# Optimization experiments

Hardware: AMD Instinct MI355X
Metric: run time of the kernel (lower is better)

Reference implementation:

```python
import jax, jax.numpy as jnp
import numpy as np

B, D, H4, L, T, VOCAB, DMID = 256, 512, 2048, 3, 201, 128, 1024
START_IDX = 0


def setup_inputs() -> dict:
    key = jax.random.key(0)
    ks = jax.random.split(key, 8)
    s = lambda k, shape, scale=0.02: jax.random.normal(k, shape, jnp.float32) * scale
    return {
        "feat": jax.random.normal(ks[0], (B, D), jnp.float32),
        "Wvis": s(ks[1], (D, D)),
        "bvis": jnp.zeros((D,), jnp.float32),
        "embed": s(ks[2], (VOCAB, D)),
        "Wih": s(ks[3], (L, H4, D)),
        "Whh": s(ks[4], (L, H4, D)),
        "bih": jnp.zeros((L, H4), jnp.float32),
        "bhh": jnp.zeros((L, H4), jnp.float32),
        "W1": s(ks[5], (DMID, D)),
        "b1": jnp.zeros((DMID,), jnp.float32),
        "W2": s(ks[6], (VOCAB, DMID)),
        "b2": jnp.zeros((VOCAB,), jnp.float32),
    }


def reference(feat, Wvis, bvis, embed, Wih, Whh, bih, bhh, W1, b1, W2, b2):
    # visual_proj applied once in forward(), then again per-layer in _init_hidden
    feat_p = feat @ Wvis.T + bvis                    # [B,D]
    h0_layer = feat_p @ Wvis.T + bvis                # same for every layer
    h0 = jnp.tile(h0_layer[None], (L, 1, 1))         # [L,B,D]
    c0 = jnp.zeros_like(h0)
    inp0 = jnp.broadcast_to(embed[START_IDX], (B, D))  # embed(<sos>)

    def step(carry, _):
        inp, h, c = carry
        x = inp
        hs, cs = [], []
        for l in range(L):  # small fixed layer count
            g = x @ Wih[l].T + bih[l] + h[l] @ Whh[l].T + bhh[l]  # [B,4D]
            i, f, gg, o = jnp.split(g, 4, axis=-1)  # torch gate order i,f,g,o
            c_l = jax.nn.sigmoid(f) * c[l] + jax.nn.sigmoid(i) * jnp.tanh(gg)
            h_l = jax.nn.sigmoid(o) * jnp.tanh(c_l)
            hs.append(h_l)
            cs.append(c_l)
            x = h_l
        out = x  # top-layer output; dropout is identity in eval
        # inp = out.detach() in the original loop
        return (jax.lax.stop_gradient(out), jnp.stack(hs), jnp.stack(cs)), out

    _, outs = jax.lax.scan(step, (inp0, h0, c0), None, length=T)  # [T,B,D]
    res = outs.transpose(1, 0, 2)                                 # [B,T,D]
    mid = jax.nn.gelu(res @ W1.T + b1, approximate=False)         # torch GELU is erf-exact
    logits = mid @ W2.T + b2                                      # [B,T,V]
    return logits.transpose(0, 2, 1)                              # [B,V,T]
```

## Files before the change

kernel.cpp:

```cpp
#include <hip/hip_runtime.h>

#define NB   256
#define ND   512
#define NH4  2048
#define NL   3
#define NT   201
#define NV   128
#define NMID 1024

typedef _Float16 half8 __attribute__((ext_vector_type(8)));
typedef float f32x4 __attribute__((ext_vector_type(4)));

__device__ __forceinline__ float sigf(float x) { return 1.0f / (1.0f + __expf(-x)); }
__device__ __forceinline__ float tanh_(float x) {
  float e = __expf(-2.0f * fabsf(x));
  float t = (1.0f - e) / (1.0f + e);
  return x < 0.0f ? -t : t;
}

__device__ __forceinline__ half8 l2_load(const _Float16* p) {
  half8 v;
  asm volatile("global_load_dwordx4 %0, %1, off sc0" : "=v"(v) : "v"(p));
  return v;
}

__device__ __forceinline__ unsigned l2_rmw_add(unsigned* p, unsigned val) {
  unsigned v;
  asm volatile("global_atomic_add %0, %1, %2, off sc0\n\ts_waitcnt vmcnt(0)"
               : "=v"(v) : "v"(p), "v"(val) : "memory");
  return v;
}

__device__ __forceinline__ void xbar(unsigned* cnt, bool pref) {
  if (pref && threadIdx.x >= 256)
    asm volatile("s_waitcnt vmcnt(8)" ::: "memory");
  else
    asm volatile("s_waitcnt vmcnt(0)" ::: "memory");
  __syncthreads();
  if (threadIdx.x == 0) {
    unsigned old = l2_rmw_add(cnt, 1u);
    unsigned target = (old & ~31u) + 32u;
    int guard = 1 << 16;
    while (l2_rmw_add(cnt, 0u) < target && --guard)
      __builtin_amdgcn_s_sleep(2);
  }
  __syncthreads();
  asm volatile("buffer_inv" ::: "memory");
  __builtin_amdgcn_sched_barrier(0);
}

__global__ void prep_all(const float* __restrict__ Wih, const float* __restrict__ Whh,
                         const float* __restrict__ bih, const float* __restrict__ bhh,
                         const float* __restrict__ Wvis, const float* __restrict__ feat,
                         const float* __restrict__ embed, const float* __restrict__ W1,
                         const float* __restrict__ W2,
                         _Float16* __restrict__ Wp, float* __restrict__ bp,
                         _Float16* __restrict__ Wvis16, _Float16* __restrict__ feat16,
                         _Float16* __restrict__ x0, _Float16* __restrict__ W1h,
                         _Float16* __restrict__ W2h, unsigned* __restrict__ cnt) {
  size_t idx = (size_t)blockIdx.x * 256 + threadIdx.x;
  {
    int k = (int)(idx & 1023);
    int R = (int)((idx >> 10) & 2047);
    int l = (int)(idx >> 21);
    int dt = R >> 6, g = (R >> 4) & 3, di = R & 15;
    int col = g * 512 + dt * 16 + di;
    float v = (k < 512) ? Wih[((size_t)l * NH4 + col) * ND + k]
                        : Whh[((size_t)l * NH4 + col) * ND + (k - 512)];
    Wp[idx] = (_Float16)v;
  }
  if (idx < (size_t)NL * NH4) {
    int R = (int)(idx & 2047);
    int l = (int)(idx >> 11);
    int dt = R >> 6, g = (R >> 4) & 3, di = R & 15;
    int col = g * 512 + dt * 16 + di;
    bp[idx] = bih[l * NH4 + col] + bhh[l * NH4 + col];
  }
  if (idx < 512 * 512)  Wvis16[idx] = (_Float16)Wvis[idx];
  if (idx < 256 * 512)  feat16[idx] = (_Float16)feat[idx];
  if (idx < 256 * 512)  x0[idx]     = (_Float16)embed[idx & 511];
  if (idx < 1024 * 512) W1h[idx]    = (_Float16)W1[idx];
  if (idx < 128 * 1024) W2h[idx]    = (_Float16)W2[idx];
  if (idx < 1024) cnt[idx] = 0;
}

__global__ __launch_bounds__(512, 2) void lstm_persist(
    const _Float16* __restrict__ Wp,
    const float* __restrict__ bp,
    const _Float16* __restrict__ Wvis,
    const float* __restrict__ bvis,
    const _Float16* __restrict__ feat16,
    const _Float16* __restrict__ x0,
    _Float16* __restrict__ featp,
    _Float16* __restrict__ hbuf,
    _Float16* __restrict__ res,
    unsigned* __restrict__ cntbase) {
  __shared__ _Float16 wlds[64][1024];
  __shared__ float expart[4][32][16][4];

  const int tid = threadIdx.x;
  const int lane = tid & 63, w = tid >> 6;
  const int lr = lane & 15, lg = (lane >> 4) & 3;

  unsigned xcd;
  asm volatile("s_getreg_b32 %0, hwreg(HW_REG_XCC_ID)" : "=s"(xcd));
  xcd &= 7u;

  unsigned* rank_slot = (unsigned*)&expart[0][0][0][0];
  if (tid == 0)
    *rank_slot = __hip_atomic_fetch_add(cntbase + 256 + xcd * 32, 1u,
                                        __ATOMIC_RELAXED, __HIP_MEMORY_SCOPE_AGENT);
  __syncthreads();
  const int rank = (int)(*rank_slot & 31u);
  __syncthreads();

  const int dt = rank;
  const int m0 = (int)xcd * 32;
  const int d0 = rank * 16;
  unsigned* cnt = cntbase + xcd * 32;

  #pragma unroll 4
  for (int i = 0; i < 16; ++i) {
    int G = tid + 512 * i;
    int r = G >> 7, g = G & 127;
    *(half8*)&wlds[r][(g ^ (r & 7)) * 8] =
        *(const half8*)(Wp + ((size_t)(dt * 64 + r)) * 1024 + g * 8);
  }
  half8 wreg[2][4][4];
  #pragma unroll
  for (int ly = 0; ly < 2; ++ly)
    #pragma unroll
    for (int n = 0; n < 4; ++n)
      #pragma unroll
      for (int kk = 0; kk < 4; ++kk)
        wreg[ly][n][kk] = *(const half8*)(Wp +
          ((size_t)((ly + 1) * NH4 + dt * 64 + n * 16 + lr)) * 1024 + w * 128 + kk * 32 + lg * 8);

  const int di = tid & 15, cb = (tid >> 4) & 31;
  f32x4 breg4[3];
  #pragma unroll
  for (int l = 0; l < 3; ++l)
    #pragma unroll
    for (int g = 0; g < 4; ++g)
      breg4[l][g] = bp[l * NH4 + dt * 64 + g * 16 + di];

  {
    float* xb = &expart[0][0][0][0];
    const int wm2 = w & 1, wk = w >> 1;
    #pragma unroll 1
    for (int pg = 0; pg < 2; ++pg) {
      const _Float16* A = pg ? featp : feat16;
      half8 avp[4];
      #pragma unroll
      for (int kc = 0; kc < 4; ++kc)
        avp[kc] = l2_load(A + (size_t)(m0 + wm2 * 16 + lr) * ND + wk * 128 + kc * 32 + lg * 8);
      asm volatile("s_waitcnt vmcnt(0)" ::: "memory");
      __builtin_amdgcn_sched_barrier(0);
      f32x4 pacc = {0.f, 0.f, 0.f, 0.f};
      #pragma unroll
      for (int kc = 0; kc < 4; ++kc) {
        half8 bb = *(const half8*)(Wvis + (size_t)(d0 + lr) * ND + wk * 128 + kc * 32 + lg * 8);
        pacc = __builtin_amdgcn_mfma_f32_16x16x32_f16(avp[kc], bb, pacc, 0, 0, 0);
      }
      #pragma unroll
      for (int j = 0; j < 4; ++j)
        xb[wk * 512 + (wm2 * 16 + lg * 4 + j) * 16 + lr] = pacc[j];
      __syncthreads();
      {
        int m = tid >> 4, d = tid & 15;
        float v = xb[m * 16 + d] + xb[512 + m * 16 + d] + xb[1024 + m * 16 + d]
                + xb[1536 + m * 16 + d] + bvis[d0 + d];
        _Float16 hv = (_Float16)v;
        size_t off = (size_t)(m0 + m) * ND + d0 + d;
        if (pg == 0) featp[off] = hv;
        else {
          hbuf[(size_t)(0 * 2 + 1) * (NB * ND) + off] = hv;
          hbuf[(size_t)(1 * 2 + 1) * (NB * ND) + off] = hv;
          hbuf[(size_t)(2 * 2 + 1) * (NB * ND) + off] = hv;
        }
      }
      xbar(cnt, false);
    }
  }

  float cst[3] = {0.f, 0.f, 0.f};
  const size_t aoff0 = (size_t)(m0 + lr) * ND + (size_t)(w & 3) * 128 + lg * 8;
  const size_t aoff1 = aoff0 + (size_t)16 * ND;
  half8 av0[4], av1[4];

  #pragma unroll 1
  for (int t = 0; t < NT; ++t) {
    #pragma unroll
    for (int l = 0; l < 3; ++l) {
      const _Float16* xsrc = (l == 0)
        ? ((t == 0) ? x0 : hbuf + (size_t)(2 * 2 + ((t + 1) & 1)) * (NB * ND))
        : hbuf + (size_t)((l - 1) * 2 + (t & 1)) * (NB * ND);
      const _Float16* hsrc = hbuf + (size_t)(l * 2 + ((t + 1) & 1)) * (NB * ND);
      _Float16* hdst       = hbuf + (size_t)(l * 2 + (t & 1)) * (NB * ND);

      f32x4 acc[2][4];
      #pragma unroll
      for (int m = 0; m < 2; ++m)
        #pragma unroll
        for (int n = 0; n < 4; ++n)
          acc[m][n] = (f32x4){0.f, 0.f, 0.f, 0.f};

      if (w < 4) {
        #pragma unroll
        for (int kk = 0; kk < 4; ++kk) {
          av0[kk] = l2_load(xsrc + aoff0 + kk * 32);
          av1[kk] = l2_load(xsrc + aoff1 + kk * 32);
        }
        asm volatile("s_waitcnt vmcnt(4)"
                     : "+v"(av0[0]), "+v"(av0[1]), "+v"(av1[0]), "+v"(av1[1]));
        __builtin_amdgcn_s_setprio(1);
        #pragma unroll
        for (int kk = 0; kk < 2; ++kk)
          #pragma unroll
          for (int n = 0; n < 4; ++n) {
            half8 bf;
            if (l == 0) {
              int kg = w * 16 + kk * 4 + lg;
              bf = *(const half8*)&wlds[n * 16 + lr][(kg ^ (lr & 7)) * 8];
            } else bf = wreg[l - 1][n][kk];
            acc[0][n] = __builtin_amdgcn_mfma_f32_16x16x32_f16(av0[kk], bf, acc[0][n], 0, 0, 0);
            acc[1][n] = __builtin_amdgcn_mfma_f32_16x16x32_f16(av1[kk], bf, acc[1][n], 0, 0, 0);
          }
        __builtin_amdgcn_s_setprio(0);
        asm volatile("s_waitcnt vmcnt(0)"
                     : "+v"(av0[2]), "+v"(av0[3]), "+v"(av1[2]), "+v"(av1[3]));
        __builtin_amdgcn_s_setprio(1);
        #pragma unroll
        for (int kk = 2; kk < 4; ++kk)
          #pragma unroll
          for (int n = 0; n < 4; ++n) {
            half8 bf;
            if (l == 0) {
              int kg = w * 16 + kk * 4 + lg;
              bf = *(const half8*)&wlds[n * 16 + lr][(kg ^ (lr & 7)) * 8];
            } else bf = wreg[l - 1][n][kk];
            acc[0][n] = __builtin_amdgcn_mfma_f32_16x16x32_f16(av0[kk], bf, acc[0][n], 0, 0, 0);
            acc[1][n] = __builtin_amdgcn_mfma_f32_16x16x32_f16(av1[kk], bf, acc[1][n], 0, 0, 0);
          }
        __builtin_amdgcn_s_setprio(0);
      } else {
        if (t == 0 && l == 0) {
          #pragma unroll
          for (int kk = 0; kk < 4; ++kk) {
            av0[kk] = l2_load(hsrc + aoff0 + kk * 32);
            av1[kk] = l2_load(hsrc + aoff1 + kk * 32);
          }
        }
        asm volatile("s_waitcnt vmcnt(0)"
                     : "+v"(av0[0]), "+v"(av0[1]), "+v"(av0[2]), "+v"(av0[3]),
                       "+v"(av1[0]), "+v"(av1[1]), "+v"(av1[2]), "+v"(av1[3]));
        __builtin_amdgcn_s_setprio(1);
        #pragma unroll
        for (int kk = 0; kk < 4; ++kk)
          #pragma unroll
          for (int n = 0; n < 4; ++n) {
            half8 bf;
            if (l == 0) {
              int kg = w * 16 + kk * 4 + lg;
              bf = *(const half8*)&wlds[n * 16 + lr][(kg ^ (lr & 7)) * 8];
            } else bf = wreg[l - 1][n][kk];
            acc[0][n] = __builtin_amdgcn_mfma_f32_16x16x32_f16(av0[kk], bf, acc[0][n], 0, 0, 0);
            acc[1][n] = __builtin_amdgcn_mfma_f32_16x16x32_f16(av1[kk], bf, acc[1][n], 0, 0, 0);
          }
        __builtin_amdgcn_s_setprio(0);
      }

      if (w >= 4) {
        #pragma unroll
        for (int m = 0; m < 2; ++m)
          #pragma unroll
          for (int j = 0; j < 4; ++j) {
            f32x4 v = {acc[m][0][j], acc[m][1][j], acc[m][2][j], acc[m][3][j]};
            *(f32x4*)&expart[w - 4][m * 16 + lg * 4 + j][lr][0] = v;
          }
      }
      __syncthreads();
      if (w < 4) {
        #pragma unroll
        for (int m = 0; m < 2; ++m)
          #pragma unroll
          for (int j = 0; j < 4; ++j) {
            f32x4* pp = (f32x4*)&expart[w][m * 16 + lg * 4 + j][lr][0];
            f32x4 tv = *pp;
            tv[0] += acc[m][0][j]; tv[1] += acc[m][1][j];
            tv[2] += acc[m][2][j]; tv[3] += acc[m][3][j];
            *pp = tv;
          }
      }
      __syncthreads();

      {
        f32x4 s4 = breg4[l];
        #pragma unroll
        for (int s = 0; s < 4; ++s) {
          f32x4 g = *(const f32x4*)&expart[s][cb][di][0];
          s4 += g;
        }
        float c = cst[l];
        c = sigf(s4[1]) * c + sigf(s4[0]) * tanh_(s4[2]);
        cst[l] = c;
        _Float16 hv = (_Float16)(sigf(s4[3]) * tanh_(c));
        size_t off = (size_t)(m0 + cb) * ND + d0 + di;
        hdst[off] = hv;
        if (l == 2) res[(size_t)t * (NB * ND) + off] = hv;
      }

      if (!(t == NT - 1 && l == 2)) {
        if (w >= 4) {
          const int nt2 = (l == 2) ? t + 1 : t;
          const int nl  = (l == 2) ? 0 : l + 1;
          const _Float16* nh = hbuf + (size_t)(nl * 2 + ((nt2 + 1) & 1)) * (NB * ND);
          #pragma unroll
          for (int kk = 0; kk < 4; ++kk) {
            av0[kk] = l2_load(nh + aoff0 + kk * 32);
            av1[kk] = l2_load(nh + aoff1 + kk * 32);
          }
        }
        xbar(cnt, true);
      }
    }
  }
}

__global__ __launch_bounds__(256, 2) void head_kernel(
    const _Float16* __restrict__ res,
    const _Float16* __restrict__ W1h,
    const float* __restrict__ b1,
    const _Float16* __restrict__ W2h,
    const float* __restrict__ b2,
    float* __restrict__ out) {
  const int tile = blockIdx.x;
  const int tid = threadIdx.x;
  const int lane = tid & 63, w = tid >> 6;
  const int lr = lane & 15, lg = lane >> 4;
  const int r0 = tile * 64;

  __shared__ _Float16 mid[64][128];

  f32x4 acc2[8];
  #pragma unroll
  for (int n = 0; n < 8; ++n) acc2[n] = (f32x4){0.f, 0.f, 0.f, 0.f};

  const size_t arow = (size_t)(r0 + w * 16 + lr) * ND;

  #pragma unroll 1
  for (int nc = 0; nc < 8; ++nc) {
    f32x4 acc1[8];
    #pragma unroll
    for (int n = 0; n < 8; ++n) acc1[n] = (f32x4){0.f, 0.f, 0.f, 0.f};
    #pragma unroll 2
    for (int kc = 0; kc < 16; ++kc) {
      half8 a = *(const half8*)(res + arow + kc * 32 + lg * 8);
      #pragma unroll
      for (int n = 0; n < 8; ++n) {
        half8 bb = *(const half8*)(W1h + (size_t)(nc * 128 + n * 16 + lr) * ND + kc * 32 + lg * 8);
        acc1[n] = __builtin_amdgcn_mfma_f32_16x16x32_f16(a, bb, acc1[n], 0, 0, 0);
      }
    }
    __syncthreads();
    #pragma unroll
    for (int n = 0; n < 8; ++n) {
      #pragma unroll
      for (int j = 0; j < 4; ++j) {
        int m = w * 16 + lg * 4 + j;
        int col = n * 16 + lr;
        float v = acc1[n][j] + b1[nc * 128 + col];
        v = 0.5f * v * (1.0f + erff(v * 0.7071067811865475f));
        int sw = (((col >> 3) ^ (m & 15)) << 3) + (col & 7);
        mid[m][sw] = (_Float16)v;
      }
    }
    __syncthreads();
    #pragma unroll
    for (int kc2 = 0; kc2 < 4; ++kc2) {
      int row = w * 16 + lr;
      int blk = (kc2 * 4 + lg) ^ (row & 15);
      half8 a2 = *(const half8*)(&mid[row][blk * 8]);
      #pragma unroll
      for (int n = 0; n < 8; ++n) {
        half8 bb = *(const half8*)(W2h + (size_t)(n * 16 + lr) * NMID + nc * 128 + kc2 * 32 + lg * 8);
        acc2[n] = __builtin_amdgcn_mfma_f32_16x16x32_f16(a2, bb, acc2[n], 0, 0, 0);
      }
    }
  }
  #pragma unroll
  for (int n = 0; n < 8; ++n) {
    #pragma unroll
    for (int j = 0; j < 4; ++j) {
      int r = r0 + w * 16 + lg * 4 + j;
      int b = r & 255, t = r >> 8;
      int v = n * 16 + lr;
      out[((size_t)b * NV + v) * NT + t] = acc2[n][j] + b2[v];
    }
  }
}

extern "C" void kernel_launch(void* const* d_in, const int* in_sizes, int n_in,
                              void* d_out, int out_size, void* d_ws, size_t ws_size,
                              hipStream_t stream) {
  const float* feat  = (const float*)d_in[0];
  const float* Wvis  = (const float*)d_in[1];
  const float* bvis  = (const float*)d_in[2];
  const float* embed = (const float*)d_in[3];
  const float* Wih   = (const float*)d_in[4];
  const float* Whh   = (const float*)d_in[5];
  const float* bih   = (const float*)d_in[6];
  const float* bhh   = (const float*)d_in[7];
  const float* W1    = (const float*)d_in[8];
  const float* b1    = (const float*)d_in[9];
  const float* W2    = (const float*)d_in[10];
  const float* b2    = (const float*)d_in[11];
  float* out = (float*)d_out;

  char* p = (char*)d_ws;
  _Float16* Wp     = (_Float16*)p; p += (size_t)NL * NH4 * 1024 * 2;
  _Float16* Wvis16 = (_Float16*)p; p += (size_t)512 * 512 * 2;
  _Float16* feat16 = (_Float16*)p; p += (size_t)256 * 512 * 2;
  _Float16* x0     = (_Float16*)p; p += (size_t)256 * 512 * 2;
  _Float16* featp  = (_Float16*)p; p += (size_t)256 * 512 * 2;
  _Float16* hbuf   = (_Float16*)p; p += (size_t)NL * 2 * NB * ND * 2;
  _Float16* resb   = (_Float16*)p; p += (size_t)NT * NB * ND * 2;
  _Float16* W1h    = (_Float16*)p; p += (size_t)NMID * ND * 2;
  _Float16* W2h    = (_Float16*)p; p += (size_t)NV * NMID * 2;
  float*    bp     = (float*)p;    p += (size_t)NL * NH4 * 4;
  unsigned* cnt    = (unsigned*)p; p += 4096;

  prep_all<<<24576, 256, 0, stream>>>(Wih, Whh, bih, bhh, Wvis, feat, embed, W1, W2,
                                      Wp, bp, Wvis16, feat16, x0, W1h, W2h, cnt);
  lstm_persist<<<256, 512, 0, stream>>>(Wp, bp, Wvis16, bvis, feat16, x0,
                                        featp, hbuf, resb, cnt);
  head_kernel<<<804, 256, 0, stream>>>(resb, W1h, b1, W2h, b2, out);
  (void)in_sizes; (void)n_in; (void)out_size; (void)ws_size;
}
```

Baseline: 2.829 ms.

## Relax grid-barrier waits, preload layer-0 LDS weights into registers, and back off early arrivals

The grid barrier is split so each caller chooses its own vmcnt wait. The res store now goes through inline asm so that store does not have to drain before the barrier (vmcnt 9 or 1 at layer 2). The first two k-chunks of the layer-0 weight fragments are read from LDS into registers before the barrier of the previous step, which hides LDS latency in the critical MFMA path. Blocks that arrive at the barrier early sleep briefly to cut atomic polling traffic on L2. The cost is more register pressure, and the early sleep may add latency.

```diff
diff --git a/kernel.cpp b/kernel.cpp
--- a/kernel.cpp
+++ b/kernel.cpp
@@ -31,15 +31,13 @@
   return v;
 }
 
-__device__ __forceinline__ void xbar(unsigned* cnt, bool pref) {
-  if (pref && threadIdx.x >= 256)
-    asm volatile("s_waitcnt vmcnt(8)" ::: "memory");
-  else
-    asm volatile("s_waitcnt vmcnt(0)" ::: "memory");
+__device__ __forceinline__ void xbar_core(unsigned* cnt) {
   __syncthreads();
   if (threadIdx.x == 0) {
     unsigned old = l2_rmw_add(cnt, 1u);
     unsigned target = (old & ~31u) + 32u;
+    int ahead = 31 - (int)(old & 31u);
+    if (ahead > 8) __builtin_amdgcn_s_sleep(8);
     int guard = 1 << 16;
     while (l2_rmw_add(cnt, 0u) < target && --guard)
       __builtin_amdgcn_s_sleep(2);
@@ -144,6 +142,8 @@
     for (int g = 0; g < 4; ++g)
       breg4[l][g] = bp[l * NH4 + dt * 64 + g * 16 + di];
 
+  half8 bl0[2][4];
+
   {
     float* xb = &expart[0][0][0][0];
     const int wm2 = w & 1, wk = w >> 1;
@@ -179,8 +179,19 @@
           hbuf[(size_t)(2 * 2 + 1) * (NB * ND) + off] = hv;
         }
       }
-      xbar(cnt, false);
-    }
+      asm volatile("s_waitcnt vmcnt(0)" ::: "memory");
+      xbar_core(cnt);
+    }
+  }
+
+  if (w < 4) {
+    #pragma unroll
+    for (int kk = 0; kk < 2; ++kk)
+      #pragma unroll
+      for (int n = 0; n < 4; ++n) {
+        int kg = w * 16 + kk * 4 + lg;
+        bl0[kk][n] = *(const half8*)&wlds[n * 16 + lr][(kg ^ (lr & 7)) * 8];
+      }
   }
 
   float cst[3] = {0.f, 0.f, 0.f};
@@ -216,6 +227,18 @@
         __builtin_amdgcn_s_setprio(1);
         #pragma unroll
         for (int kk = 0; kk < 2; ++kk)
+          #pragma unroll
+          for (int n = 0; n < 4; ++n) {
+            half8 bf = (l == 0) ? bl0[kk][n] : wreg[l - 1][n][kk];
+            acc[0][n] = __builtin_amdgcn_mfma_f32_16x16x32_f16(av0[kk], bf, acc[0][n], 0, 0, 0);
+            acc[1][n] = __builtin_amdgcn_mfma_f32_16x16x32_f16(av1[kk], bf, acc[1][n], 0, 0, 0);
+          }
+        __builtin_amdgcn_s_setprio(0);
+        asm volatile("s_waitcnt vmcnt(0)"
+                     : "+v"(av0[2]), "+v"(av0[3]), "+v"(av1[2]), "+v"(av1[3]));
+        __builtin_amdgcn_s_setprio(1);
+        #pragma unroll
+        for (int kk = 2; kk < 4; ++kk)
           #pragma unroll
           for (int n = 0; n < 4; ++n) {
             half8 bf;
@@ -227,11 +250,20 @@
             acc[1][n] = __builtin_amdgcn_mfma_f32_16x16x32_f16(av1[kk], bf, acc[1][n], 0, 0, 0);
           }
         __builtin_amdgcn_s_setprio(0);
+      } else {
+        if (t == 0 && l == 0) {
+          #pragma unroll
+          for (int kk = 0; kk < 4; ++kk) {
+            av0[kk] = l2_load(hsrc + aoff0 + kk * 32);
+            av1[kk] = l2_load(hsrc + aoff1 + kk * 32);
+          }
+        }
         asm volatile("s_waitcnt vmcnt(0)"
-                     : "+v"(av0[2]), "+v"(av0[3]), "+v"(av1[2]), "+v"(av1[3]));
+                     : "+v"(av0[0]), "+v"(av0[1]), "+v"(av0[2]), "+v"(av0[3]),
+                       "+v"(av1[0]), "+v"(av1[1]), "+v"(av1[2]), "+v"(av1[3]));
         __builtin_amdgcn_s_setprio(1);
         #pragma unroll
-        for (int kk = 2; kk < 4; ++kk)
+        for (int kk = 0; kk < 4; ++kk)
           #pragma unroll
           for (int n = 0; n < 4; ++n) {
             half8 bf;
@@ -243,31 +275,6 @@
             acc[1][n] = __builtin_amdgcn_mfma_f32_16x16x32_f16(av1[kk], bf, acc[1][n], 0, 0, 0);
           }
         __builtin_amdgcn_s_setprio(0);
-      } else {
-        if (t == 0 && l == 0) {
-          #pragma unroll
-          for (int kk = 0; kk < 4; ++kk) {
-            av0[kk] = l2_load(hsrc + aoff0 + kk * 32);
-            av1[kk] = l2_load(hsrc + aoff1 + kk * 32);
-          }
-        }
-        asm volatile("s_waitcnt vmcnt(0)"
-                     : "+v"(av0[0]), "+v"(av0[1]), "+v"(av0[2]), "+v"(av0[3]),
-                       "+v"(av1[0]), "+v"(av1[1]), "+v"(av1[2]), "+v"(av1[3]));
-        __builtin_amdgcn_s_setprio(1);
-        #pragma unroll
-        for (int kk = 0; kk < 4; ++kk)
-          #pragma unroll
-          for (int n = 0; n < 4; ++n) {
-            half8 bf;
-            if (l == 0) {
-              int kg = w * 16 + kk * 4 + lg;
-              bf = *(const half8*)&wlds[n * 16 + lr][(kg ^ (lr & 7)) * 8];
-            } else bf = wreg[l - 1][n][kk];
-            acc[0][n] = __builtin_amdgcn_mfma_f32_16x16x32_f16(av0[kk], bf, acc[0][n], 0, 0, 0);
-            acc[1][n] = __builtin_amdgcn_mfma_f32_16x16x32_f16(av1[kk], bf, acc[1][n], 0, 0, 0);
-          }
-        __builtin_amdgcn_s_setprio(0);
       }
 
       if (w >= 4) {
@@ -307,7 +314,12 @@
         _Float16 hv = (_Float16)(sigf(s4[3]) * tanh_(c));
         size_t off = (size_t)(m0 + cb) * ND + d0 + di;
         hdst[off] = hv;
-        if (l == 2) res[(size_t)t * (NB * ND) + off] = hv;
+        if (l == 2) {
+          unsigned hw = (unsigned)__builtin_bit_cast(unsigned short, hv);
+          _Float16* rp = res + (size_t)t * (NB * ND) + off;
+          asm volatile("global_store_short %0, %1, off"
+                       :: "v"(rp), "v"(hw) : "memory");
+        }
       }
 
       if (!(t == NT - 1 && l == 2)) {
@@ -320,8 +332,23 @@
             av0[kk] = l2_load(nh + aoff0 + kk * 32);
             av1[kk] = l2_load(nh + aoff1 + kk * 32);
           }
-        }
-        xbar(cnt, true);
+        } else if (l == 2) {
+          #pragma unroll
+          for (int kk = 0; kk < 2; ++kk)
+            #pragma unroll
+            for (int n = 0; n < 4; ++n) {
+              int kg = w * 16 + kk * 4 + lg;
+              bl0[kk][n] = *(const half8*)&wlds[n * 16 + lr][(kg ^ (lr & 7)) * 8];
+            }
+        }
+        if (l == 2) {
+          if (w >= 4) asm volatile("s_waitcnt vmcnt(9)" ::: "memory");
+          else        asm volatile("s_waitcnt vmcnt(1)" ::: "memory");
+        } else {
+          if (w >= 4) asm volatile("s_waitcnt vmcnt(8)" ::: "memory");
+          else        asm volatile("s_waitcnt vmcnt(0)" ::: "memory");
+        }
+        xbar_core(cnt);
       }
     }
   }
```

Result: slower. 3.260 ms (+15.2%).

## Retile head kernel so each wave computes a 64x64 block with register reuse

Applied to the files above, without the earlier changes.

The head GEMM kernel is restructured so that each wave computes all 64 rows against its own slice of the hidden dimension. Each loaded W1/W2 fragment is reused across 4 row tiles (4x4 MFMA blocks), where before each wave did 16 rows times 8 column tiles and every wave reloaded the whole weight set. The intermediate buffer grows to four per-wave 64x128 slabs (64KB of LDS), and the second GEMM splits the output columns across waves. The aim is to cut redundant global weight traffic in the head. The costs are higher register pressure, larger LDS use that may lower occupancy, and the fact that the head is likely a small share of total time next to the recurrent LSTM.

```diff
diff --git a/kernel.cpp b/kernel.cpp
--- a/kernel.cpp
+++ b/kernel.cpp
@@ -334,70 +334,93 @@
     const _Float16* __restrict__ W2h,
     const float* __restrict__ b2,
     float* __restrict__ out) {
-  const int tile = blockIdx.x;
   const int tid = threadIdx.x;
   const int lane = tid & 63, w = tid >> 6;
-  const int lr = lane & 15, lg = lane >> 4;
-  const int r0 = tile * 64;
-
-  __shared__ _Float16 mid[64][128];
-
-  f32x4 acc2[8];
+  const int lr = lane & 15, lg = (lane >> 4) & 3;
+  const int r0 = blockIdx.x * 64;
+
+  __shared__ _Float16 mid[4][64][128];
+
+  f32x4 acc2[4][2];
   #pragma unroll
-  for (int n = 0; n < 8; ++n) acc2[n] = (f32x4){0.f, 0.f, 0.f, 0.f};
-
-  const size_t arow = (size_t)(r0 + w * 16 + lr) * ND;
+  for (int m = 0; m < 4; ++m)
+    #pragma unroll
+    for (int n2 = 0; n2 < 2; ++n2) acc2[m][n2] = (f32x4){0.f, 0.f, 0.f, 0.f};
 
   #pragma unroll 1
-  for (int nc = 0; nc < 8; ++nc) {
-    f32x4 acc1[8];
-    #pragma unroll
-    for (int n = 0; n < 8; ++n) acc1[n] = (f32x4){0.f, 0.f, 0.f, 0.f};
-    #pragma unroll 2
-    for (int kc = 0; kc < 16; ++kc) {
-      half8 a = *(const half8*)(res + arow + kc * 32 + lg * 8);
-      #pragma unroll
-      for (int n = 0; n < 8; ++n) {
-        half8 bb = *(const half8*)(W1h + (size_t)(nc * 128 + n * 16 + lr) * ND + kc * 32 + lg * 8);
-        acc1[n] = __builtin_amdgcn_mfma_f32_16x16x32_f16(a, bb, acc1[n], 0, 0, 0);
-      }
+  for (int rr = 0; rr < 2; ++rr) {
+    const int c = rr * 4 + w;
+    #pragma unroll 1
+    for (int nh = 0; nh < 2; ++nh) {
+      f32x4 acc1[4][4];
+      #pragma unroll
+      for (int m = 0; m < 4; ++m)
+        #pragma unroll
+        for (int n = 0; n < 4; ++n) acc1[m][n] = (f32x4){0.f, 0.f, 0.f, 0.f};
+      #pragma unroll 2
+      for (int kc = 0; kc < 16; ++kc) {
+        half8 af[4];
+        #pragma unroll
+        for (int m = 0; m < 4; ++m)
+          af[m] = *(const half8*)(res + (size_t)(r0 + m * 16 + lr) * ND + kc * 32 + lg * 8);
+        #pragma unroll
+        for (int n = 0; n < 4; ++n) {
+          half8 bb = *(const half8*)(W1h +
+              (size_t)(c * 128 + nh * 64 + n * 16 + lr) * ND + kc * 32 + lg * 8);
+          #pragma unroll
+          for (int m = 0; m < 4; ++m)
+            acc1[m][n] = __builtin_amdgcn_mfma_f32_16x16x32_f16(af[m], bb, acc1[m][n], 0, 0, 0);
+        }
+      }
+      #pragma unroll
+      for (int n = 0; n < 4; ++n)
+        #pragma unroll
+        for (int m = 0; m < 4; ++m)
+          #pragma unroll
+          for (int j = 0; j < 4; ++j) {
+            int row = m * 16 + lg * 4 + j;
+            int col = nh * 64 + n * 16 + lr;
+            float v = acc1[m][n][j] + b1[c * 128 + col];
+            v = 0.5f * v * (1.0f + erff(v * 0.7071067811865475f));
+            int sw = (((col >> 3) ^ (row & 15)) << 3) + (col & 7);
+            mid[w][row][sw] = (_Float16)v;
+          }
     }
     __syncthreads();
-    #pragma unroll
-    for (int n = 0; n < 8; ++n) {
-      #pragma unroll
-      for (int j = 0; j < 4; ++j) {
-        int m = w * 16 + lg * 4 + j;
-        int col = n * 16 + lr;
-        float v = acc1[n][j] + b1[nc * 128 + col];
-        v = 0.5f * v * (1.0f + erff(v * 0.7071067811865475f));
-        int sw = (((col >> 3) ^ (m & 15)) << 3) + (col & 7);
-        mid[m][sw] = (_Float16)v;
+    #pragma unroll 1
+    for (int s = 0; s < 4; ++s) {
+      #pragma unroll
+      for (int kc2 = 0; kc2 < 4; ++kc2) {
+        half8 a2[4];
+        #pragma unroll
+        for (int m = 0; m < 4; ++m) {
+          int row = m * 16 + lr;
+          int blk = (kc2 * 4 + lg) ^ (row & 15);
+          a2[m] = *(const half8*)&mid[s][row][blk * 8];
+        }
+        #pragma unroll
+        for (int n2 = 0; n2 < 2; ++n2) {
+          half8 bb = *(const half8*)(W2h +
+              (size_t)(w * 32 + n2 * 16 + lr) * NMID + rr * 512 + s * 128 + kc2 * 32 + lg * 8);
+          #pragma unroll
+          for (int m = 0; m < 4; ++m)
+            acc2[m][n2] = __builtin_amdgcn_mfma_f32_16x16x32_f16(a2[m], bb, acc2[m][n2], 0, 0, 0);
+        }
       }
     }
     __syncthreads();
+  }
+  #pragma unroll
+  for (int n2 = 0; n2 < 2; ++n2)
     #pragma unroll
-    for (int kc2 = 0; kc2 < 4; ++kc2) {
-      int row = w * 16 + lr;
-      int blk = (kc2 * 4 + lg) ^ (row & 15);
-      half8 a2 = *(const half8*)(&mid[row][blk * 8]);
-      #pragma unroll
-      for (int n = 0; n < 8; ++n) {
-        half8 bb = *(const half8*)(W2h + (size_t)(n * 16 + lr) * NMID + nc * 128 + kc2 * 32 + lg * 8);
-        acc2[n] = __builtin_amdgcn_mfma_f32_16x16x32_f16(a2, bb, acc2[n], 0, 0, 0);
-      }
-    }
-  }
-  #pragma unroll
-  for (int n = 0; n < 8; ++n) {
-    #pragma unroll
-    for (int j = 0; j < 4; ++j) {
-      int r = r0 + w * 16 + lg * 4 + j;
-      int b = r & 255, t = r >> 8;
-      int v = n * 16 + lr;
-      out[((size_t)b * NV + v) * NT + t] = acc2[n][j] + b2[v];
-    }
-  }
+    for (int m = 0; m < 4; ++m)
+      #pragma unroll
+      for (int j = 0; j < 4; ++j) {
+        int r = r0 + m * 16 + lg * 4 + j;
+        int b = r & 255, t = r >> 8;
+        int v = w * 32 + n2 * 16 + lr;
+        out[((size_t)b * NV + v) * NT + t] = acc2[m][n2][j] + b2[v];
+      }
 }
 
 extern "C" void kernel_launch(void* const* d_in, const int* in_sizes, int n_in,
```

After: 2.359 ms. 1.2x faster.
